# Kernel optimization log

Measured on AMD Instinct MI355X. Metric: run time of the kernel, lower is better.

Reference implementation:

```python
import jax, jax.numpy as jnp
import numpy as np

N_UE = 16384
N_AP = 128
E = 2097152
D = 32

relu = jax.nn.relu


def setup_inputs():
    key = jax.random.key(0)
    ks = jax.random.split(key, 24)
    def g(i, shape, s=0.1):
        return jax.random.normal(ks[i], shape, dtype=jnp.float32) * s
    inp = {}
    inp["x_ue"] = jax.random.uniform(ks[0], (N_UE, 1), dtype=jnp.float32)
    inp["e_ua"] = g(1, (E, 2), 1.0)
    inp["e_au"] = g(2, (E, 2), 1.0)
    inp["src"] = jax.random.randint(ks[3], (E,), 0, N_UE)
    inp["dst"] = jax.random.randint(ks[4], (E,), 0, N_AP)
    # layer 1 (Ue2Ap): ue feat dim 1, ap feat dim 0, edge dim 2
    inp["Wm1_ua"] = g(5, (1 + 2, D)); inp["bm1_ua"] = jnp.zeros((D,), jnp.float32)
    inp["Wm1_au"] = g(6, (2, D));     inp["bm1_au"] = jnp.zeros((D,), jnp.float32)
    inp["Wu1_ap"] = g(7, (D, D));     inp["bu1_ap"] = jnp.zeros((D,), jnp.float32)
    inp["Wu1_ue"] = g(8, (1 + D, D)); inp["bu1_ue"] = jnp.zeros((D,), jnp.float32)
    inp["We1_ua"] = g(9, (2 * D + 2, 2));  inp["be1_ua"] = jnp.zeros((2,), jnp.float32)
    inp["We1_au"] = g(10, (2 * D + 2, 2)); inp["be1_au"] = jnp.zeros((2,), jnp.float32)
    # layers 2-4 stacked (all 32 -> 32)
    inp["Wm_ua"] = g(11, (3, D + 2, D)); inp["bm_ua"] = jnp.zeros((3, D), jnp.float32)
    inp["Wm_au"] = g(12, (3, D + 2, D)); inp["bm_au"] = jnp.zeros((3, D), jnp.float32)
    inp["Wu_ap"] = g(13, (3, 2 * D, D)); inp["bu_ap"] = jnp.zeros((3, D), jnp.float32)
    inp["Wu_ue"] = g(14, (3, 2 * D, D)); inp["bu_ue"] = jnp.zeros((3, D), jnp.float32)
    inp["We_ua"] = g(15, (3, 2 * D + 2, 2)); inp["be_ua"] = jnp.zeros((3, 2), jnp.float32)
    inp["We_au"] = g(16, (3, 2 * D + 2, 2)); inp["be_au"] = jnp.zeros((3, 2), jnp.float32)
    # power head: mlp([32,16]) + Lin(16,1) + Sigmoid
    inp["Wp1"] = g(17, (D, 16)); inp["bp1"] = jnp.zeros((16,), jnp.float32)
    inp["Wp2"] = g(18, (16, 1)); inp["bp2"] = jnp.zeros((1,), jnp.float32)
    return inp


def _het_conv(x_ue, x_ap, e_ua, e_au, src, dst,
              Wm_ua, bm_ua, Wm_au, bm_au,
              Wu_ap, bu_ap, Wu_ue, bu_ue,
              We_ua, be_ua, We_au, be_au):
    # ue -> ap: gather src ue feats + edge attr, MLP, scatter-add to ap
    f_ua = jnp.concatenate([x_ue[src], e_ua], axis=1)        # [E, d_ue+2]
    m_ua = relu(f_ua @ Wm_ua + bm_ua)                        # [E, D]
    agg_ap = jax.ops.segment_sum(m_ua, dst, num_segments=N_AP)
    # ap -> ue: ap has no features in layer 1 (dim 0)
    f_au = e_au if x_ap is None else jnp.concatenate([x_ap[dst], e_au], axis=1)
    m_au = relu(f_au @ Wm_au + bm_au)                        # [E, D]
    agg_ue = jax.ops.segment_sum(m_au, src, num_segments=N_UE)
    # node updates
    h_ap = agg_ap if x_ap is None else jnp.concatenate([x_ap, agg_ap], axis=1)
    x_ap_new = relu(h_ap @ Wu_ap + bu_ap)                    # [N_AP, D]
    x_ue_new = relu(jnp.concatenate([x_ue, agg_ue], axis=1) @ Wu_ue + bu_ue)  # [N_UE, D]
    # edge updates (keep edge_dim = 2)
    pair = jnp.concatenate([x_ue_new[src], x_ap_new[dst]], axis=1)  # [E, 2D]
    e_ua_new = relu(jnp.concatenate([pair, e_ua], axis=1) @ We_ua + be_ua)
    e_au_new = relu(jnp.concatenate([pair, e_au], axis=1) @ We_au + be_au)
    return x_ue_new, x_ap_new, e_ua_new, e_au_new


def reference(x_ue, e_ua, e_au, src, dst,
              Wm1_ua, bm1_ua, Wm1_au, bm1_au, Wu1_ap, bu1_ap, Wu1_ue, bu1_ue,
              We1_ua, be1_ua, We1_au, be1_au,
              Wm_ua, bm_ua, Wm_au, bm_au, Wu_ap, bu_ap, Wu_ue, bu_ue,
              We_ua, be_ua, We_au, be_au,
              Wp1, bp1, Wp2, bp2):
    x_ue, x_ap, e_ua, e_au = _het_conv(
        x_ue, None, e_ua, e_au, src, dst,
        Wm1_ua, bm1_ua, Wm1_au, bm1_au, Wu1_ap, bu1_ap, Wu1_ue, bu1_ue,
        We1_ua, be1_ua, We1_au, be1_au)
    for l in range(3):  # conv2, conv3, conv4
        x_ue, x_ap, e_ua, e_au = _het_conv(
            x_ue, x_ap, e_ua, e_au, src, dst,
            Wm_ua[l], bm_ua[l], Wm_au[l], bm_au[l],
            Wu_ap[l], bu_ap[l], Wu_ue[l], bu_ue[l],
            We_ua[l], be_ua[l], We_au[l], be_au[l])
    power = jax.nn.sigmoid(relu(x_ue @ Wp1 + bp1) @ Wp2 + bp2)  # [N_UE, 1]
    ue_out = jnp.concatenate([x_ue[:, :1], power], axis=1)      # [N_UE, 2]
    return ue_out, x_ap, e_ua, e_au
```

## Files before the change

### kernel.cpp

```cpp
#include <hip/hip_runtime.h>
#include <math.h>

#define N_UE 16384
#define N_AP 128
#define NE   2097152
#define NSB  512
#define EPSB (NE / NSB)
#define NQ   (N_UE / 4)
#define CHS  16
#define CHD  16
#define NEP  (NE + CHS * N_UE)
#define NCHU (NEP / CHS)
#define NEPD (NE + CHD * N_AP)
#define NCHD_AL 131328
#define SRC_BLKS (NCHU / 256)
#define DST_BLKS (NCHD_AL / 256)

#define RFL(x) __int_as_float(__builtin_amdgcn_readfirstlane(__float_as_int(x)))

__global__ __launch_bounds__(256) void init_kernel(
    const float* __restrict__ x_ue, const float* __restrict__ Wm1_ua,
    const float* __restrict__ bm1_ua, const float* __restrict__ bm1_au,
    float* __restrict__ Qua, float* __restrict__ Pau)
{
    int i = blockIdx.x * 256 + threadIdx.x;
    int d = i & 31;
    Qua[i] = fmaf(x_ue[i >> 5], Wm1_ua[d], bm1_ua[d]);
    if (i < N_AP * 32) Pau[i] = bm1_au[d];
    if (i < 32) { Qua[N_UE * 32 + i] = -1e30f; Pau[N_AP * 32 + i] = -1e30f; }
}

__global__ __launch_bounds__(256) void hist_both(
    const int* __restrict__ src, const int* __restrict__ dst,
    unsigned short* __restrict__ histS, int* __restrict__ histD)
{
    __shared__ unsigned int h32[N_UE / 2];
    __shared__ int hd[N_AP];
    const int tid = threadIdx.x, b = blockIdx.x;
    for (int i = tid; i < N_UE / 2; i += 256) h32[i] = 0u;
    if (tid < N_AP) hd[tid] = 0;
    __syncthreads();
    const int beg = b * EPSB;
    for (int e = beg + tid; e < beg + EPSB; e += 256) {
        int s = src[e];
        atomicAdd(&h32[s >> 1], 1u << ((s & 1) * 16));
        atomicAdd(&hd[dst[e]], 1);
    }
    __syncthreads();
    for (int i = tid; i < N_UE; i += 256)
        histS[(size_t)b * N_UE + i] =
            (unsigned short)((h32[i >> 1] >> ((i & 1) * 16)) & 0xffffu);
    if (tid < N_AP) histD[b * N_AP + tid] = hd[tid];
}

__global__ __launch_bounds__(256) void colscan_kernel(
    const unsigned short* __restrict__ histS,
    unsigned short* __restrict__ baseS, int* __restrict__ cnt)
{
    const int u = blockIdx.x * 256 + threadIdx.x;
    int run = 0;
    for (int b = 0; b < NSB; ++b) {
        int t = histS[(size_t)b * N_UE + u];
        baseS[(size_t)b * N_UE + u] = (unsigned short)run;
        run += t;
    }
    cnt[u] = run;
}

__global__ __launch_bounds__(256) void scan_src(
    const int* __restrict__ cnt, int* __restrict__ CU)
{
    __shared__ int ps[256];
    __shared__ int ps2[257];
    const int t = threadIdx.x;
    const int b0 = t * (N_UE / 256);
    int s = 0;
    for (int i = 0; i < N_UE / 256; ++i) s += (cnt[b0 + i] + CHS - 1) / CHS;
    ps[t] = s;
    __syncthreads();
    if (t == 0) {
        int r = 0;
        for (int i = 0; i < 256; ++i) { ps2[i] = r; r += ps[i]; }
        ps2[256] = r;
    }
    __syncthreads();
    int r = ps2[t];
    for (int i = 0; i < N_UE / 256; ++i) { CU[b0 + i] = r; r += (cnt[b0 + i] + CHS - 1) / CHS; }
    if (t == 255) CU[N_UE] = ps2[256];
}

__global__ __launch_bounds__(128) void scan_dst(
    const int* __restrict__ histD, int* __restrict__ offsD,
    int* __restrict__ CA, int* __restrict__ cntD)
{
    __shared__ int colTot[N_AP], colStart[N_AP];
    const int a = threadIdx.x;
    int run = 0;
    for (int b = 0; b < NSB; ++b) {
        offsD[b * N_AP + a] = run;
        run += histD[b * N_AP + a];
    }
    colTot[a] = run;
    cntD[a] = run;
    __syncthreads();
    if (a == 0) {
        int r = 0;
        for (int i = 0; i < N_AP; ++i) {
            CA[i] = r;
            colStart[i] = r * CHD;
            r += (colTot[i] + CHD - 1) / CHD;
        }
        CA[N_AP] = r;
    }
    __syncthreads();
    const int st = colStart[a];
    for (int b = 0; b < NSB; ++b) offsD[b * N_AP + a] += st;
}

__global__ __launch_bounds__(256) void scatter_both(
    const int* __restrict__ src, const int* __restrict__ dst,
    const float2* __restrict__ e0ua, const float2* __restrict__ e0au,
    const unsigned short* __restrict__ baseS, const int* __restrict__ CU,
    const int* __restrict__ offsD,
    int4* __restrict__ recS, int* __restrict__ invS,
    int* __restrict__ srcD, float2* __restrict__ attD, int* __restrict__ invD)
{
    __shared__ int cursor[NQ];
    __shared__ int cursord[N_AP];
    const int tid = threadIdx.x, b = blockIdx.x;
    const int beg = b * EPSB;
    if (tid < N_AP) cursord[tid] = offsD[b * N_AP + tid];
    for (int p = 0; p < 4; ++p) {
        const int lo = p * NQ;
        for (int i = tid; i < NQ; i += 256)
            cursor[i] = CU[lo + i] * CHS + (int)baseS[(size_t)b * N_UE + lo + i];
        __syncthreads();
        for (int e = beg + tid; e < beg + EPSB; e += 256) {
            int s = src[e];
            int dt = dst[e];
            if (p == 0) {
                int posd = atomicAdd(&cursord[dt], 1);
                srcD[posd] = s;
                attD[posd] = e0ua[e];
                invD[e] = posd;
            }
            if (s >= lo && s < lo + NQ) {
                int pos = atomicAdd(&cursor[s - lo], 1);
                float2 au = e0au[e];
                recS[pos] = make_int4(__float_as_int(au.x), __float_as_int(au.y), dt, e);
                invS[e] = pos;
            }
        }
        __syncthreads();
    }
}

__global__ __launch_bounds__(256) void build_map_src(
    const int* __restrict__ CU, const int* __restrict__ cnt,
    int* __restrict__ cnS, int4* __restrict__ recS)
{
    const int u = blockIdx.x * 256 + threadIdx.x;
    const int c0 = CU[u], c1 = CU[u + 1];
    for (int c = c0; c < c1; ++c) cnS[c] = u;
    int* recw = (int*)recS;
    for (int pos = c0 * CHS + cnt[u]; pos < c1 * CHS; ++pos)
        recw[pos * 4 + 2] = N_AP;
    const int gid = blockIdx.x * 256 + threadIdx.x;
    const int cend = CU[N_UE];
    for (int c = cend + gid; c < NCHU; c += N_UE) cnS[c] = -1;
}

__global__ __launch_bounds__(128) void build_map_dst(
    const int* __restrict__ CA, const int* __restrict__ cntD,
    int* __restrict__ cnD, int* __restrict__ srcD)
{
    const int a = threadIdx.x;
    const int c0 = CA[a], c1 = CA[a + 1];
    for (int c = c0; c < c1; ++c) cnD[c] = a;
    for (int pos = c0 * CHD + cntD[a]; pos < c1 * CHD; ++pos)
        srcD[pos] = N_UE;
    const int cend = CA[N_AP];
    for (int c = cend + a; c < NCHD_AL; c += 128) cnD[c] = -1;
}

template<bool EUPD>
__global__ __launch_bounds__(256) void pass_both(
    const int* __restrict__ cnS, int4* __restrict__ recS,
    const int* __restrict__ cnD, const int* __restrict__ srcD,
    float2* __restrict__ attD,
    const float2* __restrict__ RueA, const float2* __restrict__ RueB,
    const float2* __restrict__ RapA, const float2* __restrict__ RapB,
    const float* __restrict__ EcA, const float* __restrict__ EcB,
    const float* __restrict__ Qua, const float* __restrict__ Pau,
    const float* __restrict__ cu, const float* __restrict__ cw,
    float* __restrict__ partialU, float* __restrict__ partialA)
{
    if (blockIdx.x < SRC_BLKS) {
        const int ch = blockIdx.x * 256 + threadIdx.x;
        const int u = cnS[ch];
        if (u < 0) return;
        float w0v[32], w1v[32];
        #pragma unroll
        for (int d = 0; d < 32; ++d) { w0v[d] = RFL(cw[d]); w1v[d] = RFL(cw[32 + d]); }
        float d00 = 0.f, d01 = 0.f, d10 = 0.f, d11 = 0.f, rbx = 0.f, rby = 0.f;
        if constexpr (EUPD) {
            d00 = RFL(EcB[0]); d01 = RFL(EcB[1]); d10 = RFL(EcB[2]); d11 = RFL(EcB[3]);
            float2 r = RueB[u]; rbx = r.x; rby = r.y;
        }
        const float4* __restrict__ Pau4 = (const float4*)Pau;
        const int base = ch * CHS;
        float4 acc[8];
        #pragma unroll
        for (int q = 0; q < 8; ++q) acc[q] = make_float4(0.f, 0.f, 0.f, 0.f);
        #pragma unroll 4
        for (int j = 0; j < CHS; ++j) {
            int4 r4 = recS[base + j];
            int dt = r4.z;
            float2 a = make_float2(__int_as_float(r4.x), __int_as_float(r4.y));
            if constexpr (EUPD) {
                float2 rp = RapB[dt];
                float m0 = fmaxf(rbx + rp.x + a.x * d00 + a.y * d10, 0.f);
                float m1 = fmaxf(rby + rp.y + a.x * d01 + a.y * d11, 0.f);
                a = make_float2(m0, m1);
                *(float2*)&recS[base + j] = a;
            }
            const float4* pr = Pau4 + dt * 8;
            #pragma unroll
            for (int q = 0; q < 8; ++q) {
                float4 pv = pr[q];
                acc[q].x += fmaxf(fmaf(a.x, w0v[q*4+0], fmaf(a.y, w1v[q*4+0], pv.x)), 0.f);
                acc[q].y += fmaxf(fmaf(a.x, w0v[q*4+1], fmaf(a.y, w1v[q*4+1], pv.y)), 0.f);
                acc[q].z += fmaxf(fmaf(a.x, w0v[q*4+2], fmaf(a.y, w1v[q*4+2], pv.z)), 0.f);
                acc[q].w += fmaxf(fmaf(a.x, w0v[q*4+3], fmaf(a.y, w1v[q*4+3], pv.w)), 0.f);
            }
        }
        float4* pu = (float4*)(partialU + (size_t)ch * 32);
        #pragma unroll
        for (int q = 0; q < 8; ++q) pu[q] = acc[q];
    } else {
        const int ch = (blockIdx.x - SRC_BLKS) * 256 + threadIdx.x;
        const int a = cnD[ch];
        if (a < 0) return;
        float u0v[32], u1v[32];
        #pragma unroll
        for (int d = 0; d < 32; ++d) { u0v[d] = RFL(cu[d]); u1v[d] = RFL(cu[32 + d]); }
        float c00 = 0.f, c01 = 0.f, c10 = 0.f, c11 = 0.f, rax = 0.f, ray = 0.f;
        if constexpr (EUPD) {
            c00 = RFL(EcA[0]); c01 = RFL(EcA[1]); c10 = RFL(EcA[2]); c11 = RFL(EcA[3]);
            float2 r = RapA[a]; rax = r.x; ray = r.y;
        }
        const float4* __restrict__ Qua4 = (const float4*)Qua;
        const int base = ch * CHD;
        float4 acc[8];
        #pragma unroll
        for (int q = 0; q < 8; ++q) acc[q] = make_float4(0.f, 0.f, 0.f, 0.f);
        #pragma unroll 4
        for (int j = 0; j < CHD; ++j) {
            int s = srcD[base + j];
            float2 a2 = attD[base + j];
            if constexpr (EUPD) {
                float2 ru = RueA[s];
                float n0 = fmaxf(rax + ru.x + a2.x * c00 + a2.y * c10, 0.f);
                float n1 = fmaxf(ray + ru.y + a2.x * c01 + a2.y * c11, 0.f);
                a2 = make_float2(n0, n1);
                attD[base + j] = a2;
            }
            const float4* qr = Qua4 + s * 8;
            #pragma unroll
            for (int q = 0; q < 8; ++q) {
                float4 qv = qr[q];
                acc[q].x += fmaxf(fmaf(a2.x, u0v[q*4+0], fmaf(a2.y, u1v[q*4+0], qv.x)), 0.f);
                acc[q].y += fmaxf(fmaf(a2.x, u0v[q*4+1], fmaf(a2.y, u1v[q*4+1], qv.y)), 0.f);
                acc[q].z += fmaxf(fmaf(a2.x, u0v[q*4+2], fmaf(a2.y, u1v[q*4+2], qv.z)), 0.f);
                acc[q].w += fmaxf(fmaf(a2.x, u0v[q*4+3], fmaf(a2.y, u1v[q*4+3], qv.w)), 0.f);
            }
        }
        float4* pa = (float4*)(partialA + (size_t)ch * 32);
        #pragma unroll
        for (int q = 0; q < 8; ++q) pa[q] = acc[q];
    }
}

__global__ __launch_bounds__(256) void reduce_ue(
    const int* __restrict__ CU, const float* __restrict__ partialU,
    float* __restrict__ agg_ue)
{
    const int g   = (blockIdx.x * 256 + threadIdx.x) >> 5;
    const int dim = threadIdx.x & 31;
    const int c0 = CU[g], c1 = CU[g + 1];
    float acc = 0.f;
    for (int c = c0; c < c1; ++c) acc += partialU[(size_t)c * 32 + dim];
    agg_ue[g * 32 + dim] = acc;
}

__global__ __launch_bounds__(256) void final_edge(
    const int* __restrict__ src, const int* __restrict__ dst,
    const int* __restrict__ invS, const int* __restrict__ invD,
    const int4* __restrict__ recS, const float2* __restrict__ attD,
    const float2* __restrict__ RueA, const float2* __restrict__ RueB,
    const float2* __restrict__ RapA, const float2* __restrict__ RapB,
    const float* __restrict__ EcA, const float* __restrict__ EcB,
    float2* __restrict__ out_eua, float2* __restrict__ out_eau)
{
    const int e = blockIdx.x * 256 + threadIdx.x;
    const int s = src[e], dt = dst[e];
    float c00 = EcA[0], c01 = EcA[1], c10 = EcA[2], c11 = EcA[3];
    float d00 = EcB[0], d01 = EcB[1], d10 = EcB[2], d11 = EcB[3];
    float2 eua = attD[invD[e]];
    float2 eau = *(const float2*)(recS + invS[e]);
    float2 rA = RueA[s], pA = RapA[dt];
    float n0 = fmaxf(rA.x + pA.x + eua.x * c00 + eua.y * c10, 0.f);
    float n1 = fmaxf(rA.y + pA.y + eua.x * c01 + eua.y * c11, 0.f);
    float2 rB = RueB[s], pB = RapB[dt];
    float m0 = fmaxf(rB.x + pB.x + eau.x * d00 + eau.y * d10, 0.f);
    float m1 = fmaxf(rB.y + pB.y + eau.x * d01 + eau.y * d11, 0.f);
    out_eua[e] = make_float2(n0, n1);
    out_eau[e] = make_float2(m0, m1);
}

template<bool FIRST, bool LAST>
__global__ __launch_bounds__(64) void node_ue_kernel(
    const float* __restrict__ x_prev, const float* __restrict__ agg_ue,
    const float* __restrict__ Wu, const float* __restrict__ bu,
    const float* __restrict__ Wm_next, const float* __restrict__ bm_next,
    const float* __restrict__ WeUa, const float* __restrict__ WeUb,
    const float* __restrict__ Wp1, const float* __restrict__ bp1,
    const float* __restrict__ Wp2, const float* __restrict__ bp2,
    float* __restrict__ x_new, float* __restrict__ Qua_next,
    float2* __restrict__ RueA, float2* __restrict__ RueB,
    float2* __restrict__ ue_out)
{
    constexpr int KIN = FIRST ? 33 : 64;
    __shared__ float Wu_s[64 * 32];
    __shared__ float Wm_s[32 * 32];
    __shared__ float WeA_s[64], WeB_s[64];
    __shared__ float bu_s[32], bm_s[32];
    __shared__ float Wp1_s[32 * 16], bp1_s[16], Wp2_s[16];

    const int tid = threadIdx.x;
    for (int i = tid; i < KIN * 32; i += 64) Wu_s[i] = Wu[i];
    if (tid < 32) bu_s[tid] = bu[tid];
    if (!LAST) {
        for (int i = tid; i < 1024; i += 64) Wm_s[i] = Wm_next[i];
        if (tid < 32) bm_s[tid] = bm_next[tid];
    }
    { WeA_s[tid] = WeUa[tid]; WeB_s[tid] = WeUb[tid]; }
    if (LAST) {
        for (int i = tid; i < 512; i += 64) Wp1_s[i] = Wp1[i];
        if (tid < 16) { bp1_s[tid] = bp1[tid]; Wp2_s[tid] = Wp2[tid]; }
    }
    __syncthreads();

    const int u = blockIdx.x * 64 + tid;
    float in[KIN];
    if (FIRST) {
        in[0] = x_prev[u];
        #pragma unroll
        for (int k = 0; k < 32; ++k) in[1 + k] = agg_ue[u * 32 + k];
    } else {
        #pragma unroll
        for (int k = 0; k < 32; ++k) in[k] = x_prev[u * 32 + k];
        #pragma unroll
        for (int k = 0; k < 32; ++k) in[32 + k] = agg_ue[u * 32 + k];
    }
    float out[32];
    #pragma unroll
    for (int d = 0; d < 32; ++d) {
        float acc = bu_s[d];
        #pragma unroll
        for (int k = 0; k < KIN; ++k) acc = fmaf(in[k], Wu_s[k * 32 + d], acc);
        out[d] = fmaxf(acc, 0.f);
    }
    #pragma unroll
    for (int d = 0; d < 32; ++d) x_new[u * 32 + d] = out[d];
    if (!LAST) {
        #pragma unroll
        for (int d = 0; d < 32; ++d) {
            float acc = bm_s[d];
            #pragma unroll
            for (int k = 0; k < 32; ++k) acc = fmaf(out[k], Wm_s[k * 32 + d], acc);
            Qua_next[u * 32 + d] = acc;
        }
    }
    float r0 = 0.f, r1 = 0.f, s0 = 0.f, s1 = 0.f;
    #pragma unroll
    for (int k = 0; k < 32; ++k) {
        r0 = fmaf(out[k], WeA_s[k * 2],     r0);
        r1 = fmaf(out[k], WeA_s[k * 2 + 1], r1);
        s0 = fmaf(out[k], WeB_s[k * 2],     s0);
        s1 = fmaf(out[k], WeB_s[k * 2 + 1], s1);
    }
    RueA[u] = make_float2(r0, r1);
    RueB[u] = make_float2(s0, s1);
    if (LAST) {
        float z = bp2[0];
        #pragma unroll
        for (int j = 0; j < 16; ++j) {
            float h = bp1_s[j];
            #pragma unroll
            for (int k = 0; k < 32; ++k) h = fmaf(out[k], Wp1_s[k * 16 + j], h);
            z = fmaf(fmaxf(h, 0.f), Wp2_s[j], z);
        }
        float pw = 1.f / (1.f + expf(-z));
        ue_out[u] = make_float2(out[0], pw);
    }
}

template<bool FIRST, bool LAST>
__global__ __launch_bounds__(256) void node_ap_kernel(
    const float* __restrict__ partialA, const int* __restrict__ CA,
    const float* __restrict__ x_prev,
    const float* __restrict__ Wu, const float* __restrict__ bu,
    const float* __restrict__ Wm_next, const float* __restrict__ bm_next,
    const float* __restrict__ WeA, const float* __restrict__ beA,
    const float* __restrict__ WeB, const float* __restrict__ beB,
    float* __restrict__ x_new, float* __restrict__ Pau_next,
    float2* __restrict__ RapA, float2* __restrict__ RapB)
{
    __shared__ float red[256];
    __shared__ float agg_s[32];
    __shared__ float xnew_s[32];
    const int a = blockIdx.x, tid = threadIdx.x;
    const int d = tid & 31, p0 = tid >> 5;
    const int c0 = CA[a], c1 = CA[a + 1];
    float acc = 0.f;
    for (int p = c0 + p0; p < c1; p += 8)
        acc += partialA[(size_t)p * 32 + d];
    red[tid] = acc;
    __syncthreads();
    if (tid < 32) {
        float s = 0.f;
        #pragma unroll
        for (int i = 0; i < 8; ++i) s += red[i * 32 + tid];
        agg_s[tid] = s;
    }
    __syncthreads();
    if (tid < 32) {
        float acc2 = bu[d];
        if (FIRST) {
            #pragma unroll
            for (int k = 0; k < 32; ++k) acc2 = fmaf(agg_s[k], Wu[k * 32 + d], acc2);
        } else {
            #pragma unroll
            for (int k = 0; k < 32; ++k) acc2 = fmaf(x_prev[a * 32 + k], Wu[k * 32 + d], acc2);
            #pragma unroll
            for (int k = 0; k < 32; ++k) acc2 = fmaf(agg_s[k], Wu[(32 + k) * 32 + d], acc2);
        }
        float xn = fmaxf(acc2, 0.f);
        xnew_s[d] = xn;
        x_new[a * 32 + d] = xn;
    }
    __syncthreads();
    if (!LAST) {
        if (tid < 32) {
            float acc3 = bm_next[d];
            #pragma unroll
            for (int k = 0; k < 32; ++k) acc3 = fmaf(xnew_s[k], Wm_next[k * 32 + d], acc3);
            Pau_next[a * 32 + d] = acc3;
        }
    }
    if (tid == 0) {
        float q0 = beA[0], q1 = beA[1], t0 = beB[0], t1 = beB[1];
        #pragma unroll
        for (int k = 0; k < 32; ++k) {
            q0 = fmaf(xnew_s[k], WeA[k * 2],     q0);
            q1 = fmaf(xnew_s[k], WeA[k * 2 + 1], q1);
            t0 = fmaf(xnew_s[k], WeB[k * 2],     t0);
            t1 = fmaf(xnew_s[k], WeB[k * 2 + 1], t1);
        }
        RapA[a] = make_float2(q0, q1);
        RapB[a] = make_float2(t0, t1);
    }
}

extern "C" void kernel_launch(void* const* d_in, const int* in_sizes, int n_in,
                              void* d_out_v, int out_size, void* d_ws, size_t ws_size,
                              hipStream_t stream)
{
    const float*  x_ue   = (const float*)d_in[0];
    const float2* e0ua   = (const float2*)d_in[1];
    const float2* e0au   = (const float2*)d_in[2];
    const int*    src    = (const int*)d_in[3];
    const int*    dst    = (const int*)d_in[4];
    const float* Wm1_ua = (const float*)d_in[5];
    const float* bm1_ua = (const float*)d_in[6];
    const float* Wm1_au = (const float*)d_in[7];
    const float* bm1_au = (const float*)d_in[8];
    const float* Wu1_ap = (const float*)d_in[9];
    const float* bu1_ap = (const float*)d_in[10];
    const float* Wu1_ue = (const float*)d_in[11];
    const float* bu1_ue = (const float*)d_in[12];
    const float* We1_ua = (const float*)d_in[13];
    const float* be1_ua = (const float*)d_in[14];
    const float* We1_au = (const float*)d_in[15];
    const float* be1_au = (const float*)d_in[16];
    const float* Wm_ua  = (const float*)d_in[17];
    const float* bm_ua  = (const float*)d_in[18];
    const float* Wm_au  = (const float*)d_in[19];
    const float* bm_au  = (const float*)d_in[20];
    const float* Wu_ap  = (const float*)d_in[21];
    const float* bu_ap  = (const float*)d_in[22];
    const float* Wu_ue  = (const float*)d_in[23];
    const float* bu_ue  = (const float*)d_in[24];
    const float* We_ua  = (const float*)d_in[25];
    const float* be_ua  = (const float*)d_in[26];
    const float* We_au  = (const float*)d_in[27];
    const float* be_au  = (const float*)d_in[28];
    const float* Wp1    = (const float*)d_in[29];
    const float* bp1    = (const float*)d_in[30];
    const float* Wp2    = (const float*)d_in[31];
    const float* bp2    = (const float*)d_in[32];

    float*  outp    = (float*)d_out_v;
    float2* out_ue  = (float2*)outp;
    float*  out_ap  = outp + N_UE * 2;
    float2* out_eua = (float2*)(outp + N_UE * 2 + N_AP * 32);
    float2* out_eau = (float2*)(outp + N_UE * 2 + N_AP * 32 + (size_t)NE * 2);

    float* ws = (float*)d_ws;
    float* x_ueA  = ws;          ws += N_UE * 32;
    float* x_ueB  = ws;          ws += N_UE * 32;
    float* x_apA  = ws;          ws += N_AP * 32;
    float* x_apB  = ws;          ws += N_AP * 32;
    float* agg_ue = ws;          ws += N_UE * 32;
    float* Qua    = ws;          ws += (N_UE + 1) * 32;
    float* Pau    = ws;          ws += (N_AP + 1) * 32;
    float2* RueA  = (float2*)ws; ws += (N_UE + 2) * 2;
    float2* RueB  = (float2*)ws; ws += (N_UE + 2) * 2;
    float2* RapA  = (float2*)ws; ws += (N_AP + 2) * 2;
    float2* RapB  = (float2*)ws; ws += (N_AP + 2) * 2;
    int* cnt     = (int*)ws;     ws += N_UE;
    int* cntD    = (int*)ws;     ws += N_AP;
    int* CU      = (int*)ws;     ws += N_UE + 4;
    int* histD   = (int*)ws;     ws += NSB * N_AP;
    int* offsD   = (int*)ws;     ws += NSB * N_AP;
    int* CA      = (int*)ws;     ws += N_AP + 4;
    int* cnS     = (int*)ws;     ws += NCHU;
    int* cnD     = (int*)ws;     ws += NCHD_AL;
    int* invS    = (int*)ws;     ws += NE;
    int* invD    = (int*)ws;     ws += NE;
    int4* recS   = (int4*)ws;    ws += (size_t)NEP * 4;
    int* srcD    = (int*)ws;     ws += NEPD;
    float2* attD = (float2*)ws;  ws += (size_t)NEPD * 2;
    float* partialU = ws;        ws += (size_t)NCHU * 32;
    float* partialA = ws;        ws += (size_t)NCHD_AL * 32;
    unsigned short* histS = (unsigned short*)partialU;
    unsigned short* baseS = (unsigned short*)partialA;

    dim3 blk(256);

    hist_both<<<NSB, blk, 0, stream>>>(src, dst, histS, histD);
    colscan_kernel<<<N_UE / 256, blk, 0, stream>>>(histS, baseS, cnt);
    scan_src<<<1, blk, 0, stream>>>(cnt, CU);
    scan_dst<<<1, dim3(128), 0, stream>>>(histD, offsD, CA, cntD);
    scatter_both<<<NSB, blk, 0, stream>>>(src, dst, e0ua, e0au, baseS, CU, offsD,
                                          recS, invS, srcD, attD, invD);
    build_map_src<<<N_UE / 256, blk, 0, stream>>>(CU, cnt, cnS, recS);
    build_map_dst<<<1, dim3(128), 0, stream>>>(CA, cntD, cnD, srcD);

    init_kernel<<<N_UE * 32 / 256, blk, 0, stream>>>(x_ue, Wm1_ua, bm1_ua, bm1_au, Qua, Pau);

    const int PB = SRC_BLKS + DST_BLKS;

    pass_both<false><<<PB, blk, 0, stream>>>(
        cnS, recS, cnD, srcD, attD,
        nullptr, nullptr, nullptr, nullptr, nullptr, nullptr,
        Qua, Pau, Wm1_ua + 32, Wm1_au, partialU, partialA);
    reduce_ue<<<N_UE * 32 / 256, blk, 0, stream>>>(CU, partialU, agg_ue);
    node_ue_kernel<true, false><<<N_UE / 64, dim3(64), 0, stream>>>(
        x_ue, agg_ue, Wu1_ue, bu1_ue, Wm_ua, bm_ua, We1_ua, We1_au,
        nullptr, nullptr, nullptr, nullptr,
        x_ueA, Qua, RueA, RueB, nullptr);
    node_ap_kernel<true, false><<<N_AP, blk, 0, stream>>>(
        partialA, CA, nullptr, Wu1_ap, bu1_ap, Wm_au, bm_au,
        We1_ua + 64, be1_ua, We1_au + 64, be1_au,
        x_apA, Pau, RapA, RapB);

    pass_both<true><<<PB, blk, 0, stream>>>(
        cnS, recS, cnD, srcD, attD,
        RueA, RueB, RapA, RapB, We1_ua + 128, We1_au + 128,
        Qua, Pau, Wm_ua + 1024, Wm_au + 1024, partialU, partialA);
    reduce_ue<<<N_UE * 32 / 256, blk, 0, stream>>>(CU, partialU, agg_ue);
    node_ue_kernel<false, false><<<N_UE / 64, dim3(64), 0, stream>>>(
        x_ueA, agg_ue, Wu_ue, bu_ue, Wm_ua + 1088, bm_ua + 32, We_ua, We_au,
        nullptr, nullptr, nullptr, nullptr,
        x_ueB, Qua, RueA, RueB, nullptr);
    node_ap_kernel<false, false><<<N_AP, blk, 0, stream>>>(
        partialA, CA, x_apA, Wu_ap, bu_ap, Wm_au + 1088, bm_au + 32,
        We_ua + 64, be_ua, We_au + 64, be_au,
        x_apB, Pau, RapA, RapB);

    pass_both<true><<<PB, blk, 0, stream>>>(
        cnS, recS, cnD, srcD, attD,
        RueA, RueB, RapA, RapB, We_ua + 128, We_au + 128,
        Qua, Pau, Wm_ua + 2112, Wm_au + 2112, partialU, partialA);
    reduce_ue<<<N_UE * 32 / 256, blk, 0, stream>>>(CU, partialU, agg_ue);
    node_ue_kernel<false, false><<<N_UE / 64, dim3(64), 0, stream>>>(
        x_ueB, agg_ue, Wu_ue + 2048, bu_ue + 32, Wm_ua + 2176, bm_ua + 64,
        We_ua + 132, We_au + 132,
        nullptr, nullptr, nullptr, nullptr,
        x_ueA, Qua, RueA, RueB, nullptr);
    node_ap_kernel<false, false><<<N_AP, blk, 0, stream>>>(
        partialA, CA, x_apB, Wu_ap + 2048, bu_ap + 32, Wm_au + 2176, bm_au + 64,
        We_ua + 196, be_ua + 2, We_au + 196, be_au + 2,
        x_apA, Pau, RapA, RapB);

    pass_both<true><<<PB, blk, 0, stream>>>(
        cnS, recS, cnD, srcD, attD,
        RueA, RueB, RapA, RapB, We_ua + 260, We_au + 260,
        Qua, Pau, Wm_ua + 3200, Wm_au + 3200, partialU, partialA);
    reduce_ue<<<N_UE * 32 / 256, blk, 0, stream>>>(CU, partialU, agg_ue);
    node_ue_kernel<false, true><<<N_UE / 64, dim3(64), 0, stream>>>(
        x_ueA, agg_ue, Wu_ue + 4096, bu_ue + 64, nullptr, nullptr,
        We_ua + 264, We_au + 264,
        Wp1, bp1, Wp2, bp2,
        x_ueB, nullptr, RueA, RueB, out_ue);
    node_ap_kernel<false, true><<<N_AP, blk, 0, stream>>>(
        partialA, CA, x_apA, Wu_ap + 4096, bu_ap + 64, nullptr, nullptr,
        We_ua + 328, be_ua + 4, We_au + 328, be_au + 4,
        out_ap, nullptr, RapA, RapB);

    final_edge<<<NE / 256, blk, 0, stream>>>(
        src, dst, invS, invD, recS, attD,
        RueA, RueB, RapA, RapB,
        We_ua + 392, We_au + 392, out_eua, out_eau);
}
```

Baseline: 1.064 ms.

## Split source edge records into SoA arrays and halve source chunk size

Replaces the 16-byte int4 per-edge record (attr, dst, edge id) in the source-sorted list with separate dst index and float2 attribute arrays, dropping the unused edge-id field. Each pass now reads 12 bytes per edge instead of 16. The source chunk size drops from 16 to 8 and the inner loop is fully unrolled, which gives more threads per UE and less padding, at the cost of more partial sums for reduce_ue to read. The workspace layout is reshuffled so baseS moves inside the partialU region.

```diff
diff --git a/kernel.cpp b/kernel.cpp
--- a/kernel.cpp
+++ b/kernel.cpp
@@ -7,7 +7,7 @@
 #define NSB  512
 #define EPSB (NE / NSB)
 #define NQ   (N_UE / 4)
-#define CHS  16
+#define CHS  8
 #define CHD  16
 #define NEP  (NE + CHS * N_UE)
 #define NCHU (NEP / CHS)
@@ -122,7 +122,7 @@
     const float2* __restrict__ e0ua, const float2* __restrict__ e0au,
     const unsigned short* __restrict__ baseS, const int* __restrict__ CU,
     const int* __restrict__ offsD,
-    int4* __restrict__ recS, int* __restrict__ invS,
+    int* __restrict__ dtS, float2* __restrict__ attS, int* __restrict__ invS,
     int* __restrict__ srcD, float2* __restrict__ attD, int* __restrict__ invD)
 {
     __shared__ int cursor[NQ];
@@ -146,8 +146,8 @@
             }
             if (s >= lo && s < lo + NQ) {
                 int pos = atomicAdd(&cursor[s - lo], 1);
-                float2 au = e0au[e];
-                recS[pos] = make_int4(__float_as_int(au.x), __float_as_int(au.y), dt, e);
+                dtS[pos] = dt;
+                attS[pos] = e0au[e];
                 invS[e] = pos;
             }
         }
@@ -157,14 +157,13 @@
 
 __global__ __launch_bounds__(256) void build_map_src(
     const int* __restrict__ CU, const int* __restrict__ cnt,
-    int* __restrict__ cnS, int4* __restrict__ recS)
+    int* __restrict__ cnS, int* __restrict__ dtS)
 {
     const int u = blockIdx.x * 256 + threadIdx.x;
     const int c0 = CU[u], c1 = CU[u + 1];
     for (int c = c0; c < c1; ++c) cnS[c] = u;
-    int* recw = (int*)recS;
     for (int pos = c0 * CHS + cnt[u]; pos < c1 * CHS; ++pos)
-        recw[pos * 4 + 2] = N_AP;
+        dtS[pos] = N_AP;
     const int gid = blockIdx.x * 256 + threadIdx.x;
     const int cend = CU[N_UE];
     for (int c = cend + gid; c < NCHU; c += N_UE) cnS[c] = -1;
@@ -185,7 +184,8 @@
 
 template<bool EUPD>
 __global__ __launch_bounds__(256) void pass_both(
-    const int* __restrict__ cnS, int4* __restrict__ recS,
+    const int* __restrict__ cnS, const int* __restrict__ dtS,
+    float2* __restrict__ attS,
     const int* __restrict__ cnD, const int* __restrict__ srcD,
     float2* __restrict__ attD,
     const float2* __restrict__ RueA, const float2* __restrict__ RueB,
@@ -212,17 +212,16 @@
         float4 acc[8];
         #pragma unroll
         for (int q = 0; q < 8; ++q) acc[q] = make_float4(0.f, 0.f, 0.f, 0.f);
-        #pragma unroll 4
+        #pragma unroll
         for (int j = 0; j < CHS; ++j) {
-            int4 r4 = recS[base + j];
-            int dt = r4.z;
-            float2 a = make_float2(__int_as_float(r4.x), __int_as_float(r4.y));
+            int dt = dtS[base + j];
+            float2 a = attS[base + j];
             if constexpr (EUPD) {
                 float2 rp = RapB[dt];
                 float m0 = fmaxf(rbx + rp.x + a.x * d00 + a.y * d10, 0.f);
                 float m1 = fmaxf(rby + rp.y + a.x * d01 + a.y * d11, 0.f);
                 a = make_float2(m0, m1);
-                *(float2*)&recS[base + j] = a;
+                attS[base + j] = a;
             }
             const float4* pr = Pau4 + dt * 8;
             #pragma unroll
@@ -296,7 +295,7 @@
 __global__ __launch_bounds__(256) void final_edge(
     const int* __restrict__ src, const int* __restrict__ dst,
     const int* __restrict__ invS, const int* __restrict__ invD,
-    const int4* __restrict__ recS, const float2* __restrict__ attD,
+    const float2* __restrict__ attS, const float2* __restrict__ attD,
     const float2* __restrict__ RueA, const float2* __restrict__ RueB,
     const float2* __restrict__ RapA, const float2* __restrict__ RapB,
     const float* __restrict__ EcA, const float* __restrict__ EcB,
@@ -307,7 +306,7 @@
     float c00 = EcA[0], c01 = EcA[1], c10 = EcA[2], c11 = EcA[3];
     float d00 = EcB[0], d01 = EcB[1], d10 = EcB[2], d11 = EcB[3];
     float2 eua = attD[invD[e]];
-    float2 eau = *(const float2*)(recS + invS[e]);
+    float2 eau = attS[invS[e]];
     float2 rA = RueA[s], pA = RapA[dt];
     float n0 = fmaxf(rA.x + pA.x + eua.x * c00 + eua.y * c10, 0.f);
     float n1 = fmaxf(rA.y + pA.y + eua.x * c01 + eua.y * c11, 0.f);
@@ -539,13 +538,14 @@
     int* cnD     = (int*)ws;     ws += NCHD_AL;
     int* invS    = (int*)ws;     ws += NE;
     int* invD    = (int*)ws;     ws += NE;
-    int4* recS   = (int4*)ws;    ws += (size_t)NEP * 4;
+    int* dtS     = (int*)ws;     ws += NEP;
     int* srcD    = (int*)ws;     ws += NEPD;
+    float2* attS = (float2*)ws;  ws += (size_t)NEP * 2;
     float2* attD = (float2*)ws;  ws += (size_t)NEPD * 2;
     float* partialU = ws;        ws += (size_t)NCHU * 32;
     float* partialA = ws;        ws += (size_t)NCHD_AL * 32;
     unsigned short* histS = (unsigned short*)partialU;
-    unsigned short* baseS = (unsigned short*)partialA;
+    unsigned short* baseS = (unsigned short*)(partialU + (size_t)(NSB * N_UE / 2));
 
     dim3 blk(256);
 
@@ -554,8 +554,8 @@
     scan_src<<<1, blk, 0, stream>>>(cnt, CU);
     scan_dst<<<1, dim3(128), 0, stream>>>(histD, offsD, CA, cntD);
     scatter_both<<<NSB, blk, 0, stream>>>(src, dst, e0ua, e0au, baseS, CU, offsD,
-                                          recS, invS, srcD, attD, invD);
-    build_map_src<<<N_UE / 256, blk, 0, stream>>>(CU, cnt, cnS, recS);
+                                          dtS, attS, invS, srcD, attD, invD);
+    build_map_src<<<N_UE / 256, blk, 0, stream>>>(CU, cnt, cnS, dtS);
     build_map_dst<<<1, dim3(128), 0, stream>>>(CA, cntD, cnD, srcD);
 
     init_kernel<<<N_UE * 32 / 256, blk, 0, stream>>>(x_ue, Wm1_ua, bm1_ua, bm1_au, Qua, Pau);
@@ -563,7 +563,7 @@
     const int PB = SRC_BLKS + DST_BLKS;
 
     pass_both<false><<<PB, blk, 0, stream>>>(
-        cnS, recS, cnD, srcD, attD,
+        cnS, dtS, attS, cnD, srcD, attD,
         nullptr, nullptr, nullptr, nullptr, nullptr, nullptr,
         Qua, Pau, Wm1_ua + 32, Wm1_au, partialU, partialA);
     reduce_ue<<<N_UE * 32 / 256, blk, 0, stream>>>(CU, partialU, agg_ue);
@@ -577,7 +577,7 @@
         x_apA, Pau, RapA, RapB);
 
     pass_both<true><<<PB, blk, 0, stream>>>(
-        cnS, recS, cnD, srcD, attD,
+        cnS, dtS, attS, cnD, srcD, attD,
         RueA, RueB, RapA, RapB, We1_ua + 128, We1_au + 128,
         Qua, Pau, Wm_ua + 1024, Wm_au + 1024, partialU, partialA);
     reduce_ue<<<N_UE * 32 / 256, blk, 0, stream>>>(CU, partialU, agg_ue);
@@ -591,7 +591,7 @@
         x_apB, Pau, RapA, RapB);
 
     pass_both<true><<<PB, blk, 0, stream>>>(
-        cnS, recS, cnD, srcD, attD,
+        cnS, dtS, attS, cnD, srcD, attD,
         RueA, RueB, RapA, RapB, We_ua + 128, We_au + 128,
         Qua, Pau, Wm_ua + 2112, Wm_au + 2112, partialU, partialA);
     reduce_ue<<<N_UE * 32 / 256, blk, 0, stream>>>(CU, partialU, agg_ue);
@@ -606,7 +606,7 @@
         x_apA, Pau, RapA, RapB);
 
     pass_both<true><<<PB, blk, 0, stream>>>(
-        cnS, recS, cnD, srcD, attD,
+        cnS, dtS, attS, cnD, srcD, attD,
         RueA, RueB, RapA, RapB, We_ua + 260, We_au + 260,
         Qua, Pau, Wm_ua + 3200, Wm_au + 3200, partialU, partialA);
     reduce_ue<<<N_UE * 32 / 256, blk, 0, stream>>>(CU, partialU, agg_ue);
@@ -621,7 +621,7 @@
         out_ap, nullptr, RapA, RapB);
 
     final_edge<<<NE / 256, blk, 0, stream>>>(
-        src, dst, invS, invD, recS, attD,
+        src, dst, invS, invD, attS, attD,
         RueA, RueB, RapA, RapB,
         We_ua + 392, We_au + 392, out_eua, out_eau);
 }
```

Result: faster. 965.3 us (-9.3%).
